# Kernel optimization log

Measured on AMD Instinct MI355X. Metric: run time of the kernel, lower is better.

Reference implementation:

```python
import jax, jax.numpy as jnp
import numpy as np

# Config: 4 sparse batch items, each with 2048 active voxels (uniform-length case
# of sparse full self-attention). channels=1024, heads=16, head_dim=64.
B_SEQ, L, H, D = 4, 2048, 16, 64
C = H * D  # 1024
N = B_SEQ * L  # 8192
EPS = 1e-12  # F.normalize eps


def setup_inputs() -> dict:
    key = jax.random.key(0)
    ks = jax.random.split(key, 6)
    s = 1.0 / np.sqrt(C)
    return {
        "x": jax.random.normal(ks[0], (N, C), dtype=jnp.float32),
        "W_qkv": jax.random.normal(ks[1], (C, 3 * C), dtype=jnp.float32) * s,
        "b_qkv": jnp.zeros((3 * C,), dtype=jnp.float32),
        "gamma_q": jnp.ones((H, D), dtype=jnp.float32),
        "gamma_k": jnp.ones((H, D), dtype=jnp.float32),
        "W_out": jax.random.normal(ks[2], (C, C), dtype=jnp.float32) * s,
        "b_out": jnp.zeros((C,), dtype=jnp.float32),
    }


def _qk_rms_norm(t, gamma):
    # SparseMultiHeadRMSNorm: L2-normalize last dim, scale by gamma[h,d] * sqrt(D)
    norm = jnp.maximum(jnp.linalg.norm(t, axis=-1, keepdims=True), EPS)
    return (t / norm) * gamma * (D ** 0.5)


def reference(x, W_qkv, b_qkv, gamma_q, gamma_k, W_out, b_out):
    qkv = x @ W_qkv + b_qkv                       # [N, 3C]
    qkv = qkv.reshape(B_SEQ, L, 3, H, D)          # fused pre-reshape
    q, k, v = qkv[:, :, 0], qkv[:, :, 1], qkv[:, :, 2]  # [B,L,H,D]
    q = _qk_rms_norm(q, gamma_q)
    k = _qk_rms_norm(k, gamma_k)
    # full scaled dot-product attention within each sparse batch item
    scores = jnp.einsum('blhd,bmhd->bhlm', q, k) / (D ** 0.5)
    attn = jax.nn.softmax(scores, axis=-1)
    h = jnp.einsum('bhlm,bmhd->blhd', attn, v)    # [B,L,H,D]
    h = h.reshape(N, C)
    return h @ W_out + b_out
```

## Files before the change

kernel.cpp:

```cpp
#include <hip/hip_runtime.h>

using u16 = unsigned short;

typedef float  f32x4  __attribute__((ext_vector_type(4)));
typedef float  f32x16 __attribute__((ext_vector_type(16)));
typedef __bf16 bf16x8 __attribute__((ext_vector_type(8)));
typedef short  s16x8  __attribute__((ext_vector_type(8)));

#define DEVI __device__ __forceinline__

constexpr int TOK = 8192;
constexpr int CIN = 1024;
constexpr int C3  = 3072;
constexpr int NH  = 16;
constexpr int HD  = 64;
constexpr int SL  = 2048;
constexpr int BH  = 64;

constexpr float LOG2E = 1.4426950408889634f;

DEVI u16 f2bf(float x) {
  unsigned u = __builtin_bit_cast(unsigned, x);
  u += 0x7FFFu + ((u >> 16) & 1u);
  return (u16)(u >> 16);
}

DEVI f32x4 mfma16(s16x8 a, s16x8 b, f32x4 c) {
  return __builtin_amdgcn_mfma_f32_16x16x32_bf16(
      __builtin_bit_cast(bf16x8, a), __builtin_bit_cast(bf16x8, b), c, 0, 0, 0);
}

DEVI f32x16 mfma32(s16x8 a, s16x8 b, f32x16 c) {
  return __builtin_amdgcn_mfma_f32_32x32x16_bf16(
      __builtin_bit_cast(bf16x8, a), __builtin_bit_cast(bf16x8, b), c, 0, 0, 0);
}

DEVI void gload_lds16(const void* g, void* l) {
  __builtin_amdgcn_global_load_lds(
      (const __attribute__((address_space(1))) unsigned int*)g,
      (__attribute__((address_space(3))) unsigned int*)l, 16, 0, 0);
}

DEVI unsigned cvtpk(float lo, float hi) {
  unsigned r;
  asm("v_cvt_pk_bf16_f32 %0, %1, %2" : "=v"(r) : "v"(lo), "v"(hi));
  return r;
}

DEVI void plswap(unsigned& a, unsigned& b) {
  asm("v_permlane32_swap_b32 %0, %1" : "+v"(a), "+v"(b));
}

__global__ __launch_bounds__(256) void k_cvt_x(const float* __restrict__ x,
                                               u16* __restrict__ xb) {
  const int total = TOK * CIN / 4;
  for (int i = blockIdx.x * 256 + threadIdx.x; i < total; i += gridDim.x * 256) {
    float4 v = ((const float4*)x)[i];
    ushort4 o;
    o.x = f2bf(v.x); o.y = f2bf(v.y); o.z = f2bf(v.z); o.w = f2bf(v.w);
    ((ushort4*)xb)[i] = o;
  }
}

__global__ __launch_bounds__(256) void k_transpose(const float* __restrict__ in,
                                                   u16* __restrict__ out,
                                                   int R, int C) {
  __shared__ u16 t[64][72];
  int rt = R >> 6;
  int tr = (blockIdx.x % rt) << 6;
  int tc = (blockIdx.x / rt) << 6;
  int tid = threadIdx.x;
#pragma unroll
  for (int k2 = 0; k2 < 16; k2++) {
    int idx = k2 * 256 + tid;
    int r = idx >> 6, c = idx & 63;
    t[r][c] = f2bf(in[(size_t)(tr + r) * C + tc + c]);
  }
  __syncthreads();
#pragma unroll
  for (int k2 = 0; k2 < 16; k2++) {
    int idx = k2 * 256 + tid;
    int r = idx >> 6, c = idx & 63;
    out[(size_t)(tc + r) * R + tr + c] = t[c][r];
  }
}

#define STAGE6(BUF, KT)                                                  \
  { char* Ld = L + (BUF) * 49152;                                        \
    const size_t ko = (size_t)(KT) * 128;                                \
    gload_lds16(Ab + ko,          Ld + wb);                              \
    gload_lds16(Ab + ko + 131072, Ld + 8192 + wb);                       \
    gload_lds16(Ab + ko + 262144, Ld + 16384 + wb);                      \
    gload_lds16(Ab + ko + 393216, Ld + 24576 + wb);                      \
    gload_lds16(Bb + ko,          Ld + 32768 + wb);                      \
    gload_lds16(Bb + ko + 131072, Ld + 40960 + wb); }

#define KBODY(KT, DOSTAGE, VMSTR)                                        \
  {                                                                      \
    if (DOSTAGE) STAGE6(((KT) + 2) % 3, (KT) + 2)                        \
    asm volatile("s_waitcnt " VMSTR ::: "memory");                       \
    __builtin_amdgcn_s_barrier();                                        \
    const char* Lb = L + ((KT) % 3) * 49152;                             \
    s16x8 af[4][2], bfr[4][2];                                           \
    _Pragma("unroll")                                                    \
    for (int mf = 0; mf < 4; mf++) {                                     \
      af[mf][0] = *(const s16x8*)(Lb + aoff + mf * 2048 + cx0);          \
      af[mf][1] = *(const s16x8*)(Lb + aoff + mf * 2048 + (cx0 ^ 64));   \
    }                                                                    \
    _Pragma("unroll")                                                    \
    for (int nf = 0; nf < 4; nf++) {                                     \
      bfr[nf][0] = *(const s16x8*)(Lb + boff + nf * 2048 + cx0);         \
      bfr[nf][1] = *(const s16x8*)(Lb + boff + nf * 2048 + (cx0 ^ 64));  \
    }                                                                    \
    __builtin_amdgcn_s_setprio(1);                                       \
    _Pragma("unroll")                                                    \
    for (int ks = 0; ks < 2; ks++)                                       \
      _Pragma("unroll")                                                  \
      for (int mf = 0; mf < 4; mf++)                                     \
        _Pragma("unroll")                                                \
        for (int nf = 0; nf < 4; nf++)                                   \
          acc[mf][nf] = mfma16(af[mf][ks], bfr[nf][ks], acc[mf][nf]);    \
    __builtin_amdgcn_s_setprio(0);                                       \
    __builtin_amdgcn_s_barrier();                                        \
  }

DEVI void gemm_mainloop(const char* Ab, const char* Bb, char* L,
                        int wb, int aoff, int boff, int cx0,
                        f32x4 (&acc)[4][4]) {
  STAGE6(0, 0)
  STAGE6(1, 1)
#pragma unroll
  for (int kt = 0; kt < 14; ++kt) KBODY(kt, 1, "vmcnt(12)")
  KBODY(14, 0, "vmcnt(6)")
  KBODY(15, 0, "vmcnt(0)")
}

__global__ __launch_bounds__(512, 2) void k_gemm_qkv(
    const u16* __restrict__ A, const u16* __restrict__ Bt,
    const float* __restrict__ bias, const float* __restrict__ gq,
    const float* __restrict__ gk,
    u16* __restrict__ Qn, u16* __restrict__ Kn, u16* __restrict__ Vt) {
  __shared__ __align__(16) char Lsh[3][49152];
  int bid = blockIdx.x;
  bid = (bid & 7) * 96 + (bid >> 3);
  const int bm = (bid / 24) * 256, bn = (bid % 24) * 128;
  const int tid = threadIdx.x, lane = tid & 63, w = tid >> 6;
  const int l15 = lane & 15, g = lane >> 4;
  const int wr4 = w >> 1, wc2 = w & 1;

  const int rA  = tid >> 3;
  const int scb = ((tid & 7) << 4) ^ ((rA & 7) << 4);
  const char* Ab = (const char*)A + (size_t)(bm + rA) * 2048 + scb;
  const char* Bb = (const char*)Bt + (size_t)(bn + rA) * 2048 + scb;
  const int wb   = w << 10;
  const int aoff = (wr4 * 64 + l15) * 128;
  const int boff = 32768 + (wc2 * 64 + l15) * 128;
  const int cx0  = (g ^ (l15 & 7)) << 4;

  f32x4 acc[4][4];
#pragma unroll
  for (int i = 0; i < 4; i++)
#pragma unroll
    for (int j = 0; j < 4; j++) acc[i][j] = f32x4{0.f, 0.f, 0.f, 0.f};

  gemm_mainloop(Ab, Bb, (char*)Lsh, wb, aoff, boff, cx0, acc);

  const int c0 = bn + wc2 * 64;
  const int sec = c0 >> 10;
  const int head = (c0 & 1023) >> 6;
  float bv[4], gv[4];
#pragma unroll
  for (int nf = 0; nf < 4; nf++) {
    bv[nf] = bias[c0 + nf * 16 + l15];
    gv[nf] = 1.f;
    if (sec == 0) gv[nf] = gq[head * 64 + nf * 16 + l15];
    if (sec == 1) gv[nf] = gk[head * 64 + nf * 16 + l15];
  }
#pragma unroll
  for (int mf = 0; mf < 4; mf++) {
#pragma unroll
    for (int nf = 0; nf < 4; nf++)
#pragma unroll
      for (int r = 0; r < 4; r++) acc[mf][nf][r] += bv[nf];
    if (sec < 2) {
#pragma unroll
      for (int r = 0; r < 4; r++) {
        float ss = 0.f;
#pragma unroll
        for (int nf = 0; nf < 4; nf++) ss += acc[mf][nf][r] * acc[mf][nf][r];
        ss += __shfl_xor(ss, 1); ss += __shfl_xor(ss, 2);
        ss += __shfl_xor(ss, 4); ss += __shfl_xor(ss, 8);
        float nrm = fmaxf(sqrtf(ss), 1e-12f);
        float f = (sec == 0 ? LOG2E : 8.0f) / nrm;
#pragma unroll
        for (int nf = 0; nf < 4; nf++) acc[mf][nf][r] *= f;
      }
    }
    int rbase = bm + wr4 * 64 + mf * 16 + 4 * g;
#pragma unroll
    for (int r = 0; r < 4; r++) {
      int row = rbase + r;
      int b = row >> 11, tok = row & 2047;
      int bh = b * NH + head;
#pragma unroll
      for (int nf = 0; nf < 4; nf++) {
        int d = nf * 16 + l15;
        u16 val = f2bf(acc[mf][nf][r] * gv[nf]);
        if (sec == 0)      Qn[((size_t)bh * SL + tok) * HD + d] = val;
        else if (sec == 1) Kn[((size_t)bh * SL + tok) * HD + d] = val;
        else               Vt[((size_t)bh * HD + d) * SL + tok] = val;
      }
    }
  }
}

__global__ __launch_bounds__(512, 2) void k_gemm_out(
    const u16* __restrict__ A, const u16* __restrict__ Bt,
    const float* __restrict__ bias, float* __restrict__ out) {
  __shared__ __align__(16) char Lsh[3][49152];
  int bid = blockIdx.x;
  bid = (bid & 7) * 32 + (bid >> 3);
  const int bm = (bid / 8) * 256, bn = (bid % 8) * 128;
  const int tid = threadIdx.x, lane = tid & 63, w = tid >> 6;
  const int l15 = lane & 15, g = lane >> 4;
  const int wr4 = w >> 1, wc2 = w & 1;

  const int rA  = tid >> 3;
  const int scb = ((tid & 7) << 4) ^ ((rA & 7) << 4);
  const char* Ab = (const char*)A + (size_t)(bm + rA) * 2048 + scb;
  const char* Bb = (const char*)Bt + (size_t)(bn + rA) * 2048 + scb;
  const int wb   = w << 10;
  const int aoff = (wr4 * 64 + l15) * 128;
  const int boff = 32768 + (wc2 * 64 + l15) * 128;
  const int cx0  = (g ^ (l15 & 7)) << 4;

  f32x4 acc[4][4];
#pragma unroll
  for (int i = 0; i < 4; i++)
#pragma unroll
    for (int j = 0; j < 4; j++) acc[i][j] = f32x4{0.f, 0.f, 0.f, 0.f};

  gemm_mainloop(Ab, Bb, (char*)Lsh, wb, aoff, boff, cx0, acc);

  float bv[4];
#pragma unroll
  for (int nf = 0; nf < 4; nf++) bv[nf] = bias[bn + wc2 * 64 + nf * 16 + l15];
#pragma unroll
  for (int mf = 0; mf < 4; mf++)
#pragma unroll
    for (int r = 0; r < 4; r++) {
      int row = bm + wr4 * 64 + mf * 16 + 4 * g + r;
#pragma unroll
      for (int nf = 0; nf < 4; nf++)
        out[(size_t)row * CIN + bn + wc2 * 64 + nf * 16 + l15] =
            acc[mf][nf][r] + bv[nf];
    }
}

__global__ __launch_bounds__(512) void k_attn(const u16* __restrict__ Qn,
                                              const u16* __restrict__ Kn,
                                              const u16* __restrict__ Vt,
                                              u16* __restrict__ hm) {
  __shared__ __align__(16) char KL[2][8192];
  __shared__ __align__(16) char VL[2][8192];
  const int bh = blockIdx.x & 63, qb = blockIdx.x >> 6;
  const int tid = threadIdx.x, w = tid >> 6, lane = tid & 63;
  const int l31 = lane & 31, h = lane >> 5;
  const int qr0 = qb * 256 + w * 32;

  const int sr  = tid >> 3;
  const int scb = ((tid & 7) << 4) ^ ((sr & 7) << 4);
  const char* kst = (const char*)(Kn + (size_t)bh * SL * HD) + (size_t)sr * 128 + scb;
  const char* vst = (const char*)(Vt + (size_t)bh * HD * SL) + (size_t)sr * 4096 + scb;
  char* kl0 = KL[0] + (w << 10);
  char* vl0 = VL[0] + (w << 10);
  char* kl1 = KL[1] + (w << 10);
  char* vl1 = VL[1] + (w << 10);

  const u16* Qb = Qn + ((size_t)bh * SL + qr0 + l31) * HD + 8 * h;
  s16x8 qf[4];
#pragma unroll
  for (int ks = 0; ks < 4; ks++) qf[ks] = *(const s16x8*)(Qb + ks * 16);

  const int lb = l31 * 128 + ((h << 4) ^ ((l31 & 7) << 4));

  f32x16 o0, o1;
#pragma unroll
  for (int i = 0; i < 16; i++) { o0[i] = 0.f; o1[i] = 0.f; }
  float mr = -1e30f, lr = 0.f;

  gload_lds16(kst, kl0);
  gload_lds16(vst, vl0);
  __syncthreads();

  for (int it = 0; it < 32; ++it) {
    const char* KB = (it & 1) ? KL[1] : KL[0];
    const char* VB = (it & 1) ? VL[1] : VL[0];
    if (it < 31) {
      const size_t ko = (size_t)(it + 1) << 13;
      const size_t vo = (size_t)(it + 1) << 7;
      gload_lds16(kst + ko, (it & 1) ? kl0 : kl1);
      gload_lds16(vst + vo, (it & 1) ? vl0 : vl1);
    }

    f32x16 s0, s1;
#pragma unroll
    for (int i = 0; i < 16; i++) { s0[i] = 0.f; s1[i] = 0.f; }
    __builtin_amdgcn_s_setprio(1);
#pragma unroll
    for (int ks = 0; ks < 4; ks++) {
      const s16x8 ka  = *(const s16x8*)(KB + (lb ^ (ks << 5)));
      const s16x8 kb2 = *(const s16x8*)(KB + 4096 + (lb ^ (ks << 5)));
      s0 = mfma32(ka, qf[ks], s0);
      s1 = mfma32(kb2, qf[ks], s1);
    }
    __builtin_amdgcn_s_setprio(0);

    float mx8[8];
#pragma unroll
    for (int i = 0; i < 8; i++)
      mx8[i] = fmaxf(fmaxf(s0[i], s0[i + 8]), fmaxf(s1[i], s1[i + 8]));
    float m0 = fmaxf(fmaxf(mx8[0], mx8[1]), fmaxf(mx8[2], mx8[3]));
    float m1 = fmaxf(fmaxf(mx8[4], mx8[5]), fmaxf(mx8[6], mx8[7]));
    float bm = fmaxf(m0, m1);
    bm = fmaxf(bm, __shfl_xor(bm, 32));

    if (!__all(bm <= mr + 8.f)) {
      const float mn = fmaxf(mr, bm);
      const float sc = __builtin_amdgcn_exp2f(mr - mn);
      mr = mn;
      lr *= sc;
#pragma unroll
      for (int i = 0; i < 16; i++) { o0[i] *= sc; o1[i] *= sc; }
    }
#pragma unroll
    for (int i = 0; i < 16; i++) s0[i] = __builtin_amdgcn_exp2f(s0[i] - mr);
#pragma unroll
    for (int i = 0; i < 16; i++) s1[i] = __builtin_amdgcn_exp2f(s1[i] - mr);
    float sm8[8];
#pragma unroll
    for (int i = 0; i < 8; i++)
      sm8[i] = (s0[i] + s0[i + 8]) + (s1[i] + s1[i + 8]);
    lr += ((sm8[0] + sm8[1]) + (sm8[2] + sm8[3])) +
          ((sm8[4] + sm8[5]) + (sm8[6] + sm8[7]));

    union PBu { unsigned u[4]; s16x8 v; } pb;
#define MK_PB(SV, B)                              \
    {                                             \
      unsigned a0 = cvtpk(SV[B + 0], SV[B + 1]);  \
      unsigned c0 = cvtpk(SV[B + 4], SV[B + 5]);  \
      plswap(a0, c0);                             \
      unsigned a1 = cvtpk(SV[B + 2], SV[B + 3]);  \
      unsigned c1 = cvtpk(SV[B + 6], SV[B + 7]);  \
      plswap(a1, c1);                             \
      pb.u[0] = a0; pb.u[1] = a1; pb.u[2] = c0; pb.u[3] = c1; \
    }
#define PV_STEP(KS)                                            \
    {                                                          \
      const s16x8 va = *(const s16x8*)(VB + (lb ^ (KS << 5))); \
      const s16x8 vb = *(const s16x8*)(VB + 4096 + (lb ^ (KS << 5))); \
      __builtin_amdgcn_s_setprio(1);                           \
      o0 = mfma32(va, pb.v, o0);                               \
      o1 = mfma32(vb, pb.v, o1);                               \
      __builtin_amdgcn_s_setprio(0);                           \
    }
    MK_PB(s0, 0) PV_STEP(0)
    MK_PB(s0, 8) PV_STEP(1)
    MK_PB(s1, 0) PV_STEP(2)
    MK_PB(s1, 8) PV_STEP(3)
#undef MK_PB
#undef PV_STEP

    __syncthreads();
  }

  const float ltot = lr + __shfl_xor(lr, 32);
  const float inv = 1.f / ltot;
  const int bq = bh >> 4, hh = bh & 15;
  u16* hb = hm + ((size_t)bq * SL + qr0 + l31) * CIN + hh * HD;
#pragma unroll
  for (int rg = 0; rg < 4; rg++) {
    const int d0 = 8 * rg + 4 * h;
    unsigned lo = cvtpk(o0[4 * rg + 0] * inv, o0[4 * rg + 1] * inv);
    unsigned hi = cvtpk(o0[4 * rg + 2] * inv, o0[4 * rg + 3] * inv);
    *(unsigned long long*)(hb + d0) =
        (unsigned long long)lo | ((unsigned long long)hi << 32);
    unsigned lo1 = cvtpk(o1[4 * rg + 0] * inv, o1[4 * rg + 1] * inv);
    unsigned hi1 = cvtpk(o1[4 * rg + 2] * inv, o1[4 * rg + 3] * inv);
    *(unsigned long long*)(hb + 32 + d0) =
        (unsigned long long)lo1 | ((unsigned long long)hi1 << 32);
  }
}

extern "C" void kernel_launch(void* const* d_in, const int* in_sizes, int n_in,
                              void* d_out, int out_size, void* d_ws, size_t ws_size,
                              hipStream_t stream) {
  const float* x    = (const float*)d_in[0];
  const float* Wqkv = (const float*)d_in[1];
  const float* bqkv = (const float*)d_in[2];
  const float* gq   = (const float*)d_in[3];
  const float* gk   = (const float*)d_in[4];
  const float* Wout = (const float*)d_in[5];
  const float* bout = (const float*)d_in[6];
  float* out = (float*)d_out;

  char* ws = (char*)d_ws;
  u16* xb  = (u16*)(ws);
  u16* wqT = (u16*)(ws + 16777216);
  u16* woT = (u16*)(ws + 23068672);
  u16* Qn  = (u16*)(ws + 25165824);
  u16* Kn  = (u16*)(ws + 41943040);
  u16* Vt  = (u16*)(ws + 58720256);
  u16* hm  = (u16*)(ws + 75497472);

  k_cvt_x<<<2048, 256, 0, stream>>>(x, xb);
  k_transpose<<<(1024 / 64) * (3072 / 64), 256, 0, stream>>>(Wqkv, wqT, 1024, 3072);
  k_transpose<<<(1024 / 64) * (1024 / 64), 256, 0, stream>>>(Wout, woT, 1024, 1024);
  k_gemm_qkv<<<(TOK / 256) * (C3 / 128), 512, 0, stream>>>(xb, wqT, bqkv, gq, gk, Qn, Kn, Vt);
  k_attn<<<BH * (SL / 256), 512, 0, stream>>>(Qn, Kn, Vt, hm);
  k_gemm_out<<<(TOK / 256) * (CIN / 128), 512, 0, stream>>>(hm, woT, bout, out);
}
```

Measured before the change: 209.9 us.

## Have each attention wave process two 32-row query tiles sharing K/V fragments

The attention block shrinks from 8 to 4 waves, and each wave now owns 64 query rows split into two 32-row tiles (A and B). K and V fragments are loaded from LDS once per iteration and reused by both tiles' MFMAs, which halves LDS reads per query row and gives each wave more independent MFMA work. Each thread now stages two K and two V chunks per tile. This raises register pressure (four output accumulators plus prefetched K/V fragments), which may lower occupancy, and leaves fewer waves per block to hide latency.

Result: slower. 251.7 us (+19.9%).

```diff
diff --git a/kernel.cpp b/kernel.cpp
--- a/kernel.cpp
+++ b/kernel.cpp
@@ -257,7 +257,7 @@
     }
 }
 
-__global__ __launch_bounds__(512) void k_attn(const u16* __restrict__ Qn,
+__global__ __launch_bounds__(256) void k_attn(const u16* __restrict__ Qn,
                                               const u16* __restrict__ Kn,
                                               const u16* __restrict__ Vt,
                                               u16* __restrict__ hm) {
@@ -266,83 +266,102 @@
   const int bh = blockIdx.x & 63, qb = blockIdx.x >> 6;
   const int tid = threadIdx.x, w = tid >> 6, lane = tid & 63;
   const int l31 = lane & 31, h = lane >> 5;
-  const int qr0 = qb * 256 + w * 32;
-
-  const int sr  = tid >> 3;
-  const int scb = ((tid & 7) << 4) ^ ((sr & 7) << 4);
-  const char* kst = (const char*)(Kn + (size_t)bh * SL * HD) + (size_t)sr * 128 + scb;
-  const char* vst = (const char*)(Vt + (size_t)bh * HD * SL) + (size_t)sr * 4096 + scb;
-  char* kl0 = KL[0] + (w << 10);
-  char* vl0 = VL[0] + (w << 10);
-  char* kl1 = KL[1] + (w << 10);
-  char* vl1 = VL[1] + (w << 10);
-
-  const u16* Qb = Qn + ((size_t)bh * SL + qr0 + l31) * HD + 8 * h;
-  s16x8 qf[4];
-#pragma unroll
-  for (int ks = 0; ks < 4; ks++) qf[ks] = *(const s16x8*)(Qb + ks * 16);
+  const int qr0 = qb * 256 + w * 64;
+
+  const int sr0 = (w << 4) + (lane >> 3);
+  const int scb = (((lane & 7) << 4)) ^ ((((lane >> 3) & 7)) << 4);
+  const char* kst = (const char*)(Kn + (size_t)bh * SL * HD) + (size_t)sr0 * 128 + scb;
+  const char* vst = (const char*)(Vt + (size_t)bh * HD * SL) + (size_t)sr0 * 4096 + scb;
+
+#define STAGE_A(BUF, IT)                                                   \
+  { char* kd = KL[BUF] + (w << 11); char* vd = VL[BUF] + (w << 11);        \
+    const size_t ko = (size_t)(IT) << 13;             \
+    const size_t vo = (size_t)(IT) << 7;               \
+    gload_lds16(kst + ko,         kd);                                     \
+    gload_lds16(kst + ko + 1024,  kd + 1024);                              \
+    gload_lds16(vst + vo,         vd);                                     \
+    gload_lds16(vst + vo + 32768, vd + 1024); }
+
+  const u16* QbA = Qn + ((size_t)bh * SL + qr0 + l31) * HD + 8 * h;
+  s16x8 qfA[4], qfB[4];
+#pragma unroll
+  for (int ks = 0; ks < 4; ks++) {
+    qfA[ks] = *(const s16x8*)(QbA + ks * 16);
+    qfB[ks] = *(const s16x8*)(QbA + 32 * HD + ks * 16);
+  }
 
   const int lb = l31 * 128 + ((h << 4) ^ ((l31 & 7) << 4));
 
-  f32x16 o0, o1;
-#pragma unroll
-  for (int i = 0; i < 16; i++) { o0[i] = 0.f; o1[i] = 0.f; }
-  float mr = -1e30f, lr = 0.f;
-
-  gload_lds16(kst, kl0);
-  gload_lds16(vst, vl0);
+  f32x16 oA0, oA1, oB0, oB1;
+#pragma unroll
+  for (int i = 0; i < 16; i++) { oA0[i] = 0.f; oA1[i] = 0.f; oB0[i] = 0.f; oB1[i] = 0.f; }
+  float mrA = -1e30f, lrA = 0.f, mrB = -1e30f, lrB = 0.f;
+
+  STAGE_A(0, 0)
   __syncthreads();
 
   for (int it = 0; it < 32; ++it) {
     const char* KB = (it & 1) ? KL[1] : KL[0];
     const char* VB = (it & 1) ? VL[1] : VL[0];
-    if (it < 31) {
-      const size_t ko = (size_t)(it + 1) << 13;
-      const size_t vo = (size_t)(it + 1) << 7;
-      gload_lds16(kst + ko, (it & 1) ? kl0 : kl1);
-      gload_lds16(vst + vo, (it & 1) ? vl0 : vl1);
-    }
-
-    f32x16 s0, s1;
-#pragma unroll
-    for (int i = 0; i < 16; i++) { s0[i] = 0.f; s1[i] = 0.f; }
+    if (it < 31) STAGE_A(it & 1 ? 0 : 1, it + 1)
+
+    s16x8 kf[4][2];
+#pragma unroll
+    for (int ks = 0; ks < 4; ks++) {
+      kf[ks][0] = *(const s16x8*)(KB + (lb ^ (ks << 5)));
+      kf[ks][1] = *(const s16x8*)(KB + 4096 + (lb ^ (ks << 5)));
+    }
+    f32x16 sA0, sA1, sB0, sB1;
+#pragma unroll
+    for (int i = 0; i < 16; i++) { sA0[i] = 0.f; sA1[i] = 0.f; sB0[i] = 0.f; sB1[i] = 0.f; }
     __builtin_amdgcn_s_setprio(1);
 #pragma unroll
     for (int ks = 0; ks < 4; ks++) {
-      const s16x8 ka  = *(const s16x8*)(KB + (lb ^ (ks << 5)));
-      const s16x8 kb2 = *(const s16x8*)(KB + 4096 + (lb ^ (ks << 5)));
-      s0 = mfma32(ka, qf[ks], s0);
-      s1 = mfma32(kb2, qf[ks], s1);
+      sA0 = mfma32(kf[ks][0], qfA[ks], sA0);
+      sA1 = mfma32(kf[ks][1], qfA[ks], sA1);
+      sB0 = mfma32(kf[ks][0], qfB[ks], sB0);
+      sB1 = mfma32(kf[ks][1], qfB[ks], sB1);
     }
     __builtin_amdgcn_s_setprio(0);
 
-    float mx8[8];
-#pragma unroll
-    for (int i = 0; i < 8; i++)
-      mx8[i] = fmaxf(fmaxf(s0[i], s0[i + 8]), fmaxf(s1[i], s1[i + 8]));
-    float m0 = fmaxf(fmaxf(mx8[0], mx8[1]), fmaxf(mx8[2], mx8[3]));
-    float m1 = fmaxf(fmaxf(mx8[4], mx8[5]), fmaxf(mx8[6], mx8[7]));
-    float bm = fmaxf(m0, m1);
-    bm = fmaxf(bm, __shfl_xor(bm, 32));
-
-    if (!__all(bm <= mr + 8.f)) {
-      const float mn = fmaxf(mr, bm);
-      const float sc = __builtin_amdgcn_exp2f(mr - mn);
-      mr = mn;
-      lr *= sc;
-#pragma unroll
-      for (int i = 0; i < 16; i++) { o0[i] *= sc; o1[i] *= sc; }
-    }
-#pragma unroll
-    for (int i = 0; i < 16; i++) s0[i] = __builtin_amdgcn_exp2f(s0[i] - mr);
-#pragma unroll
-    for (int i = 0; i < 16; i++) s1[i] = __builtin_amdgcn_exp2f(s1[i] - mr);
-    float sm8[8];
-#pragma unroll
-    for (int i = 0; i < 8; i++)
-      sm8[i] = (s0[i] + s0[i + 8]) + (s1[i] + s1[i + 8]);
-    lr += ((sm8[0] + sm8[1]) + (sm8[2] + sm8[3])) +
-          ((sm8[4] + sm8[5]) + (sm8[6] + sm8[7]));
+    s16x8 vf[4][2];
+#pragma unroll
+    for (int ks = 0; ks < 4; ks++) {
+      vf[ks][0] = *(const s16x8*)(VB + (lb ^ (ks << 5)));
+      vf[ks][1] = *(const s16x8*)(VB + 4096 + (lb ^ (ks << 5)));
+    }
+
+#define SMAX(S0, S1, MR, LR, O0, O1)                                        \
+    {                                                                       \
+      float mx8[8];                                                         \
+      _Pragma("unroll")                                                     \
+      for (int i = 0; i < 8; i++)                                           \
+        mx8[i] = fmaxf(fmaxf(S0[i], S0[i + 8]), fmaxf(S1[i], S1[i + 8]));   \
+      float m0 = fmaxf(fmaxf(mx8[0], mx8[1]), fmaxf(mx8[2], mx8[3]));       \
+      float m1 = fmaxf(fmaxf(mx8[4], mx8[5]), fmaxf(mx8[6], mx8[7]));       \
+      float bm = fmaxf(m0, m1);                                             \
+      bm = fmaxf(bm, __shfl_xor(bm, 32));                                   \
+      if (!__all(bm <= MR + 8.f)) {                                         \
+        const float mn = fmaxf(MR, bm);                                     \
+        const float sc = __builtin_amdgcn_exp2f(MR - mn);                   \
+        MR = mn; LR *= sc;                                                  \
+        _Pragma("unroll")                                                   \
+        for (int i = 0; i < 16; i++) { O0[i] *= sc; O1[i] *= sc; }          \
+      }                                                                     \
+      _Pragma("unroll")                                                     \
+      for (int i = 0; i < 16; i++) S0[i] = __builtin_amdgcn_exp2f(S0[i] - MR); \
+      _Pragma("unroll")                                                     \
+      for (int i = 0; i < 16; i++) S1[i] = __builtin_amdgcn_exp2f(S1[i] - MR); \
+      float sm8[8];                                                         \
+      _Pragma("unroll")                                                     \
+      for (int i = 0; i < 8; i++)                                           \
+        sm8[i] = (S0[i] + S0[i + 8]) + (S1[i] + S1[i + 8]);                 \
+      LR += ((sm8[0] + sm8[1]) + (sm8[2] + sm8[3])) +                       \
+            ((sm8[4] + sm8[5]) + (sm8[6] + sm8[7]));                        \
+    }
+    SMAX(sA0, sA1, mrA, lrA, oA0, oA1)
+    SMAX(sB0, sB1, mrB, lrB, oB0, oB1)
+#undef SMAX
 
     union PBu { unsigned u[4]; s16x8 v; } pb;
 #define MK_PB(SV, B)                              \
@@ -355,41 +374,63 @@
       plswap(a1, c1);                             \
       pb.u[0] = a0; pb.u[1] = a1; pb.u[2] = c0; pb.u[3] = c1; \
     }
-#define PV_STEP(KS)                                            \
+#define PV_STEP(KS, O0, O1)                                    \
     {                                                          \
-      const s16x8 va = *(const s16x8*)(VB + (lb ^ (KS << 5))); \
-      const s16x8 vb = *(const s16x8*)(VB + 4096 + (lb ^ (KS << 5))); \
       __builtin_amdgcn_s_setprio(1);                           \
-      o0 = mfma32(va, pb.v, o0);                               \
-      o1 = mfma32(vb, pb.v, o1);                               \
+      O0 = mfma32(vf[KS][0], pb.v, O0);                        \
+      O1 = mfma32(vf[KS][1], pb.v, O1);                        \
       __builtin_amdgcn_s_setprio(0);                           \
     }
-    MK_PB(s0, 0) PV_STEP(0)
-    MK_PB(s0, 8) PV_STEP(1)
-    MK_PB(s1, 0) PV_STEP(2)
-    MK_PB(s1, 8) PV_STEP(3)
+    MK_PB(sA0, 0) PV_STEP(0, oA0, oA1)
+    MK_PB(sA0, 8) PV_STEP(1, oA0, oA1)
+    MK_PB(sA1, 0) PV_STEP(2, oA0, oA1)
+    MK_PB(sA1, 8) PV_STEP(3, oA0, oA1)
+    MK_PB(sB0, 0) PV_STEP(0, oB0, oB1)
+    MK_PB(sB0, 8) PV_STEP(1, oB0, oB1)
+    MK_PB(sB1, 0) PV_STEP(2, oB0, oB1)
+    MK_PB(sB1, 8) PV_STEP(3, oB0, oB1)
 #undef MK_PB
 #undef PV_STEP
 
     __syncthreads();
   }
 
-  const float ltot = lr + __shfl_xor(lr, 32);
-  const float inv = 1.f / ltot;
   const int bq = bh >> 4, hh = bh & 15;
-  u16* hb = hm + ((size_t)bq * SL + qr0 + l31) * CIN + hh * HD;
-#pragma unroll
-  for (int rg = 0; rg < 4; rg++) {
-    const int d0 = 8 * rg + 4 * h;
-    unsigned lo = cvtpk(o0[4 * rg + 0] * inv, o0[4 * rg + 1] * inv);
-    unsigned hi = cvtpk(o0[4 * rg + 2] * inv, o0[4 * rg + 3] * inv);
-    *(unsigned long long*)(hb + d0) =
-        (unsigned long long)lo | ((unsigned long long)hi << 32);
-    unsigned lo1 = cvtpk(o1[4 * rg + 0] * inv, o1[4 * rg + 1] * inv);
-    unsigned hi1 = cvtpk(o1[4 * rg + 2] * inv, o1[4 * rg + 3] * inv);
-    *(unsigned long long*)(hb + 32 + d0) =
-        (unsigned long long)lo1 | ((unsigned long long)hi1 << 32);
-  }
+  {
+    const float ltot = lrA + __shfl_xor(lrA, 32);
+    const float inv = 1.f / ltot;
+    u16* hb = hm + ((size_t)bq * SL + qr0 + l31) * CIN + hh * HD;
+#pragma unroll
+    for (int rg = 0; rg < 4; rg++) {
+      const int d0 = 8 * rg + 4 * h;
+      unsigned lo = cvtpk(oA0[4 * rg + 0] * inv, oA0[4 * rg + 1] * inv);
+      unsigned hi = cvtpk(oA0[4 * rg + 2] * inv, oA0[4 * rg + 3] * inv);
+      *(unsigned long long*)(hb + d0) =
+          (unsigned long long)lo | ((unsigned long long)hi << 32);
+      unsigned lo1 = cvtpk(oA1[4 * rg + 0] * inv, oA1[4 * rg + 1] * inv);
+      unsigned hi1 = cvtpk(oA1[4 * rg + 2] * inv, oA1[4 * rg + 3] * inv);
+      *(unsigned long long*)(hb + 32 + d0) =
+          (unsigned long long)lo1 | ((unsigned long long)hi1 << 32);
+    }
+  }
+  {
+    const float ltot = lrB + __shfl_xor(lrB, 32);
+    const float inv = 1.f / ltot;
+    u16* hb = hm + ((size_t)bq * SL + qr0 + 32 + l31) * CIN + hh * HD;
+#pragma unroll
+    for (int rg = 0; rg < 4; rg++) {
+      const int d0 = 8 * rg + 4 * h;
+      unsigned lo = cvtpk(oB0[4 * rg + 0] * inv, oB0[4 * rg + 1] * inv);
+      unsigned hi = cvtpk(oB0[4 * rg + 2] * inv, oB0[4 * rg + 3] * inv);
+      *(unsigned long long*)(hb + d0) =
+          (unsigned long long)lo | ((unsigned long long)hi << 32);
+      unsigned lo1 = cvtpk(oB1[4 * rg + 0] * inv, oB1[4 * rg + 1] * inv);
+      unsigned hi1 = cvtpk(oB1[4 * rg + 2] * inv, oB1[4 * rg + 3] * inv);
+      *(unsigned long long*)(hb + 32 + d0) =
+          (unsigned long long)lo1 | ((unsigned long long)hi1 << 32);
+    }
+  }
+#undef STAGE_A
 }
 
 extern "C" void kernel_launch(void* const* d_in, const int* in_sizes, int n_in,
@@ -417,6 +458,6 @@
   k_transpose<<<(1024 / 64) * (3072 / 64), 256, 0, stream>>>(Wqkv, wqT, 1024, 3072);
   k_transpose<<<(1024 / 64) * (1024 / 64), 256, 0, stream>>>(Wout, woT, 1024, 1024);
   k_gemm_qkv<<<(TOK / 256) * (C3 / 128), 512, 0, stream>>>(xb, wqT, bqkv, gq, gk, Qn, Kn, Vt);
-  k_attn<<<BH * (SL / 256), 512, 0, stream>>>(Qn, Kn, Vt, hm);
+  k_attn<<<BH * (SL / 256), 256, 0, stream>>>(Qn, Kn, Vt, hm);
   k_gemm_out<<<(TOK / 256) * (CIN / 128), 512, 0, stream>>>(hm, woT, bout, out);
 }
```

## Load K/V fragments directly from global memory in attention, dropping LDS staging

Applied to the files above, without the earlier changes.

The attention kernel stops staging K and V tiles through double-buffered shared memory with block-wide barriers. Each wave now reads its MFMA operand fragments for K and V directly from global memory, relying on L2 and L1 to serve the reuse across waves. Blocks shrink to 256 threads over 128 query rows, so twice as many blocks are launched. This removes the per-iteration barriers and LDS traffic, but every wave now fetches K and V redundantly from global memory and no load is prefetched ahead of its use.

After: 365.6 us. 74.2% more time.

```diff
diff --git a/kernel.cpp b/kernel.cpp
--- a/kernel.cpp
+++ b/kernel.cpp
@@ -257,64 +257,53 @@
     }
 }
 
-__global__ __launch_bounds__(512) void k_attn(const u16* __restrict__ Qn,
+__global__ __launch_bounds__(256) void k_attn(const u16* __restrict__ Qn,
                                               const u16* __restrict__ Kn,
                                               const u16* __restrict__ Vt,
                                               u16* __restrict__ hm) {
-  __shared__ __align__(16) char KL[2][8192];
-  __shared__ __align__(16) char VL[2][8192];
   const int bh = blockIdx.x & 63, qb = blockIdx.x >> 6;
   const int tid = threadIdx.x, w = tid >> 6, lane = tid & 63;
   const int l31 = lane & 31, h = lane >> 5;
-  const int qr0 = qb * 256 + w * 32;
-
-  const int sr  = tid >> 3;
-  const int scb = ((tid & 7) << 4) ^ ((sr & 7) << 4);
-  const char* kst = (const char*)(Kn + (size_t)bh * SL * HD) + (size_t)sr * 128 + scb;
-  const char* vst = (const char*)(Vt + (size_t)bh * HD * SL) + (size_t)sr * 4096 + scb;
-  char* kl0 = KL[0] + (w << 10);
-  char* vl0 = VL[0] + (w << 10);
-  char* kl1 = KL[1] + (w << 10);
-  char* vl1 = VL[1] + (w << 10);
+  const int qr0 = qb * 128 + w * 32;
+
+  const u16* Kb = Kn + (size_t)bh * SL * HD;
+  const u16* Vb = Vt + (size_t)bh * HD * SL;
 
   const u16* Qb = Qn + ((size_t)bh * SL + qr0 + l31) * HD + 8 * h;
   s16x8 qf[4];
 #pragma unroll
   for (int ks = 0; ks < 4; ks++) qf[ks] = *(const s16x8*)(Qb + ks * 16);
 
-  const int lb = l31 * 128 + ((h << 4) ^ ((l31 & 7) << 4));
+  const u16* Ka = Kb + (size_t)l31 * HD + 8 * h;
+  const u16* Va = Vb + (size_t)l31 * SL + 8 * h;
 
   f32x16 o0, o1;
 #pragma unroll
   for (int i = 0; i < 16; i++) { o0[i] = 0.f; o1[i] = 0.f; }
   float mr = -1e30f, lr = 0.f;
 
-  gload_lds16(kst, kl0);
-  gload_lds16(vst, vl0);
-  __syncthreads();
-
   for (int it = 0; it < 32; ++it) {
-    const char* KB = (it & 1) ? KL[1] : KL[0];
-    const char* VB = (it & 1) ? VL[1] : VL[0];
-    if (it < 31) {
-      const size_t ko = (size_t)(it + 1) << 13;
-      const size_t vo = (size_t)(it + 1) << 7;
-      gload_lds16(kst + ko, (it & 1) ? kl0 : kl1);
-      gload_lds16(vst + vo, (it & 1) ? vl0 : vl1);
-    }
+    const int kb = it * 64;
 
     f32x16 s0, s1;
 #pragma unroll
     for (int i = 0; i < 16; i++) { s0[i] = 0.f; s1[i] = 0.f; }
-    __builtin_amdgcn_s_setprio(1);
 #pragma unroll
     for (int ks = 0; ks < 4; ks++) {
-      const s16x8 ka  = *(const s16x8*)(KB + (lb ^ (ks << 5)));
-      const s16x8 kb2 = *(const s16x8*)(KB + 4096 + (lb ^ (ks << 5)));
+      const s16x8 ka  = *(const s16x8*)(Ka + (size_t)kb * HD + ks * 16);
+      const s16x8 kb2 = *(const s16x8*)(Ka + (size_t)(kb + 32) * HD + ks * 16);
+      __builtin_amdgcn_s_setprio(1);
       s0 = mfma32(ka, qf[ks], s0);
       s1 = mfma32(kb2, qf[ks], s1);
-    }
-    __builtin_amdgcn_s_setprio(0);
+      __builtin_amdgcn_s_setprio(0);
+    }
+
+    s16x8 vf[4][2];
+#pragma unroll
+    for (int ks = 0; ks < 4; ks++) {
+      vf[ks][0] = *(const s16x8*)(Va + kb + ks * 16);
+      vf[ks][1] = *(const s16x8*)(Va + (size_t)32 * SL + kb + ks * 16);
+    }
 
     float mx8[8];
 #pragma unroll
@@ -357,11 +346,9 @@
     }
 #define PV_STEP(KS)                                            \
     {                                                          \
-      const s16x8 va = *(const s16x8*)(VB + (lb ^ (KS << 5))); \
-      const s16x8 vb = *(const s16x8*)(VB + 4096 + (lb ^ (KS << 5))); \
       __builtin_amdgcn_s_setprio(1);                           \
-      o0 = mfma32(va, pb.v, o0);                               \
-      o1 = mfma32(vb, pb.v, o1);                               \
+      o0 = mfma32(vf[KS][0], pb.v, o0);                        \
+      o1 = mfma32(vf[KS][1], pb.v, o1);                        \
       __builtin_amdgcn_s_setprio(0);                           \
     }
     MK_PB(s0, 0) PV_STEP(0)
@@ -370,8 +357,6 @@
     MK_PB(s1, 8) PV_STEP(3)
 #undef MK_PB
 #undef PV_STEP
-
-    __syncthreads();
   }
 
   const float ltot = lr + __shfl_xor(lr, 32);
@@ -417,6 +402,6 @@
   k_transpose<<<(1024 / 64) * (3072 / 64), 256, 0, stream>>>(Wqkv, wqT, 1024, 3072);
   k_transpose<<<(1024 / 64) * (1024 / 64), 256, 0, stream>>>(Wout, woT, 1024, 1024);
   k_gemm_qkv<<<(TOK / 256) * (C3 / 128), 512, 0, stream>>>(xb, wqT, bqkv, gq, gk, Qn, Kn, Vt);
-  k_attn<<<BH * (SL / 256), 512, 0, stream>>>(Qn, Kn, Vt, hm);
+  k_attn<<<BH * (SL / 128), 256, 0, stream>>>(Qn, Kn, Vt, hm);
   k_gemm_out<<<(TOK / 256) * (CIN / 128), 512, 0, stream>>>(hm, woT, bout, out);
 }
```

## Replace online softmax max tracking with static per-head score bound

Applied to the files above, without the earlier changes.

Because Q and K are L2-normalized and scaled by gamma*sqrt(D), each score is bounded by 8*log2e*max|gq*gk| per head. A tiny kernel computes that bound, and the attention kernel folds it into the MFMA accumulator init, removing the per-tile row max, cross-lane shuffle, and rescale of O. The bound is mathematically valid for any gamma, but exp2 may underflow when actual scores are far below the bound, which risks precision loss for large gammas. The bound buffer reuses the xb workspace after the QKV GEMM.

After: 205.1 us. 1.02x faster.

```diff
diff --git a/kernel.cpp b/kernel.cpp
--- a/kernel.cpp
+++ b/kernel.cpp
@@ -83,6 +83,24 @@
     int r = idx >> 6, c = idx & 63;
     out[(size_t)(tc + r) * R + tr + c] = t[c][r];
   }
+}
+
+__global__ __launch_bounds__(256) void k_bound(const float* __restrict__ gq,
+                                               const float* __restrict__ gk,
+                                               float* __restrict__ bnd) {
+  const int tid = threadIdx.x;
+  const int h = tid >> 4, s = tid & 15;
+  float mv = 0.f;
+#pragma unroll
+  for (int j = 0; j < 4; j++) {
+    int d = s * 4 + j;
+    mv = fmaxf(mv, fabsf(gq[h * 64 + d] * gk[h * 64 + d]));
+  }
+  mv = fmaxf(mv, __shfl_xor(mv, 1));
+  mv = fmaxf(mv, __shfl_xor(mv, 2));
+  mv = fmaxf(mv, __shfl_xor(mv, 4));
+  mv = fmaxf(mv, __shfl_xor(mv, 8));
+  if (s == 0) bnd[h] = 8.0f * LOG2E * mv;
 }
 
 #define STAGE6(BUF, KT)                                                  \
@@ -260,6 +278,7 @@
 __global__ __launch_bounds__(512) void k_attn(const u16* __restrict__ Qn,
                                               const u16* __restrict__ Kn,
                                               const u16* __restrict__ Vt,
+                                              const float* __restrict__ bnd,
                                               u16* __restrict__ hm) {
   __shared__ __align__(16) char KL[2][8192];
   __shared__ __align__(16) char VL[2][8192];
@@ -267,6 +286,7 @@
   const int tid = threadIdx.x, w = tid >> 6, lane = tid & 63;
   const int l31 = lane & 31, h = lane >> 5;
   const int qr0 = qb * 256 + w * 32;
+  const float negM = -bnd[bh & 15];
 
   const int sr  = tid >> 3;
   const int scb = ((tid & 7) << 4) ^ ((sr & 7) << 4);
@@ -287,7 +307,7 @@
   f32x16 o0, o1;
 #pragma unroll
   for (int i = 0; i < 16; i++) { o0[i] = 0.f; o1[i] = 0.f; }
-  float mr = -1e30f, lr = 0.f;
+  float lr = 0.f;
 
   gload_lds16(kst, kl0);
   gload_lds16(vst, vl0);
@@ -305,7 +325,7 @@
 
     f32x16 s0, s1;
 #pragma unroll
-    for (int i = 0; i < 16; i++) { s0[i] = 0.f; s1[i] = 0.f; }
+    for (int i = 0; i < 16; i++) { s0[i] = negM; s1[i] = negM; }
     __builtin_amdgcn_s_setprio(1);
 #pragma unroll
     for (int ks = 0; ks < 4; ks++) {
@@ -316,27 +336,10 @@
     }
     __builtin_amdgcn_s_setprio(0);
 
-    float mx8[8];
-#pragma unroll
-    for (int i = 0; i < 8; i++)
-      mx8[i] = fmaxf(fmaxf(s0[i], s0[i + 8]), fmaxf(s1[i], s1[i + 8]));
-    float m0 = fmaxf(fmaxf(mx8[0], mx8[1]), fmaxf(mx8[2], mx8[3]));
-    float m1 = fmaxf(fmaxf(mx8[4], mx8[5]), fmaxf(mx8[6], mx8[7]));
-    float bm = fmaxf(m0, m1);
-    bm = fmaxf(bm, __shfl_xor(bm, 32));
-
-    if (!__all(bm <= mr + 8.f)) {
-      const float mn = fmaxf(mr, bm);
-      const float sc = __builtin_amdgcn_exp2f(mr - mn);
-      mr = mn;
-      lr *= sc;
-#pragma unroll
-      for (int i = 0; i < 16; i++) { o0[i] *= sc; o1[i] *= sc; }
-    }
-#pragma unroll
-    for (int i = 0; i < 16; i++) s0[i] = __builtin_amdgcn_exp2f(s0[i] - mr);
-#pragma unroll
-    for (int i = 0; i < 16; i++) s1[i] = __builtin_amdgcn_exp2f(s1[i] - mr);
+#pragma unroll
+    for (int i = 0; i < 16; i++) s0[i] = __builtin_amdgcn_exp2f(s0[i]);
+#pragma unroll
+    for (int i = 0; i < 16; i++) s1[i] = __builtin_amdgcn_exp2f(s1[i]);
     float sm8[8];
 #pragma unroll
     for (int i = 0; i < 8; i++)
@@ -412,11 +415,13 @@
   u16* Kn  = (u16*)(ws + 41943040);
   u16* Vt  = (u16*)(ws + 58720256);
   u16* hm  = (u16*)(ws + 75497472);
+  float* bnd = (float*)xb;
 
   k_cvt_x<<<2048, 256, 0, stream>>>(x, xb);
   k_transpose<<<(1024 / 64) * (3072 / 64), 256, 0, stream>>>(Wqkv, wqT, 1024, 3072);
   k_transpose<<<(1024 / 64) * (1024 / 64), 256, 0, stream>>>(Wout, woT, 1024, 1024);
   k_gemm_qkv<<<(TOK / 256) * (C3 / 128), 512, 0, stream>>>(xb, wqT, bqkv, gq, gk, Qn, Kn, Vt);
-  k_attn<<<BH * (SL / 256), 512, 0, stream>>>(Qn, Kn, Vt, hm);
+  k_bound<<<1, 256, 0, stream>>>(gq, gk, bnd);
+  k_attn<<<BH * (SL / 256), 512, 0, stream>>>(Qn, Kn, Vt, bnd, hm);
   k_gemm_out<<<(TOK / 256) * (CIN / 128), 512, 0, stream>>>(hm, woT, bout, out);
 }
```
